# Performance work log

Measured on AMD Instinct MI355X. Metric: run time of the kernel, lower is better.

Reference implementation:

```python
import jax, jax.numpy as jnp
import numpy as np

# MLA dims (DeepSeek-V3-lite style)
B, S, DIM = 1, 2048, 2048
H, NOPE, ROPE, VD, LORA = 16, 128, 64, 128, 512
QK_HEAD = NOPE + ROPE  # 192
SCALE = QK_HEAD ** -0.5
EPS = 1e-6


def _rmsnorm(x, w):
    return x * jax.lax.rsqrt(jnp.mean(x * x, axis=-1, keepdims=True) + EPS) * w


def _apply_rope(x, cos, sin):
    # x: [b, s, h, d] with interleaved (real, imag) pairs; cos/sin: [s, d//2]
    x0, x1 = x[..., 0::2], x[..., 1::2]
    c = cos[None, :, None, :]
    s = sin[None, :, None, :]
    y0 = x0 * c - x1 * s
    y1 = x0 * s + x1 * c
    return jnp.stack([y0, y1], axis=-1).reshape(x.shape)


def setup_inputs() -> dict:
    key = jax.random.key(0)
    ks = jax.random.split(key, 6)
    x = jax.random.normal(ks[0], (B, S, DIM), jnp.float32) * 0.02
    wq = jax.random.normal(ks[1], (H * QK_HEAD, DIM), jnp.float32) * 0.02
    wkv_a = jax.random.normal(ks[2], (LORA + ROPE, DIM), jnp.float32) * 0.02
    kv_norm_w = jnp.ones((LORA,), jnp.float32)
    wkv_b = jax.random.normal(ks[3], (H * (NOPE + VD), LORA), jnp.float32) * 0.02
    wo = jax.random.normal(ks[4], (DIM, H * VD), jnp.float32) * 0.02
    # rotary freqs_cis (cos/sin) for qk_rope_head_dim
    inv_freq = 1.0 / (10000.0 ** (np.arange(0, ROPE, 2, dtype=np.float32) / ROPE))
    t = np.arange(S, dtype=np.float32)
    ang = np.outer(t, inv_freq)  # [S, ROPE//2]
    cos = jnp.asarray(np.cos(ang), jnp.float32)
    sin = jnp.asarray(np.sin(ang), jnp.float32)
    return {"x": x, "cos": cos, "sin": sin, "wq": wq, "wkv_a": wkv_a,
            "kv_norm_w": kv_norm_w, "wkv_b": wkv_b, "wo": wo}


def reference(x, cos, sin, wq, wkv_a, kv_norm_w, wkv_b, wo):
    b, s, _ = x.shape
    # queries
    q = (x @ wq.T).reshape(b, s, H, QK_HEAD)
    q_nope, q_pe = q[..., :NOPE], q[..., NOPE:]
    q_pe = _apply_rope(q_pe, cos, sin)  # [b,s,h,rope]
    # latent kv
    kv = x @ wkv_a.T  # [b,s,lora+rope]
    kv_c, k_pe = kv[..., :LORA], kv[..., LORA:]
    k_pe = _apply_rope(k_pe[:, :, None, :], cos, sin)[:, :, 0, :]  # [b,s,rope]
    kv_c = _rmsnorm(kv_c, kv_norm_w)  # latent kv cache [b,s,lora]
    # absorbed weights: wkv_b viewed as [h, nope+vd, lora]
    wkv_b_r = wkv_b.reshape(H, NOPE + VD, LORA)
    w_uk = wkv_b_r[:, :NOPE]   # [h, nope, lora]
    w_uv = wkv_b_r[:, NOPE:]   # [h, vd, lora]
    # absorb: project q_nope into latent space
    q_c = jnp.einsum('bshd,hdc->bshc', q_nope, w_uk)  # [b,s,h,lora]
    scores = (jnp.einsum('bshc,btc->bsht', q_c, kv_c)
              + jnp.einsum('bshr,btr->bsht', q_pe, k_pe)) * SCALE
    # causal mask over [s, t]
    mask = jnp.where(jnp.arange(s)[:, None] >= jnp.arange(s)[None, :], 0.0, -1e30)
    scores = scores + mask[None, :, None, :].astype(scores.dtype)
    attn = jax.nn.softmax(scores, axis=-1)
    o = jnp.einsum('bsht,btc->bshc', attn, kv_c)       # [b,s,h,lora]
    o = jnp.einsum('bshc,hdc->bshd', o, w_uv)           # [b,s,h,vd]
    out = o.reshape(b, s, H * VD) @ wo.T                # [b,s,dim]
    return out
```

## Files before the change

### kernel.cpp

```cpp
#include <hip/hip_runtime.h>
#include <hip/hip_bf16.h>
#include <math.h>

#define S_LEN 2048
#define DIM   2048
#define H_N   16
#define NOPE  128
#define ROPE  64
#define VD    128
#define LORA  512
#define D_QK  576
#define SCALE_F 0.07216878364870323f
#define EPS_F 1e-6f
#define KVF 640
#define KVS 1280

typedef short short8 __attribute__((ext_vector_type(8)));
typedef short short4v __attribute__((ext_vector_type(4)));
typedef float floatx4 __attribute__((ext_vector_type(4)));

static __device__ inline unsigned short f2bf_bits(float f) {
  union { __hip_bfloat16 h; unsigned short u; } cv;
  cv.h = __float2bfloat16(f);
  return cv.u;
}

static __device__ inline float bf2f(unsigned short b) {
  union { unsigned u; float f; } cv;
  cv.u = (unsigned)b << 16;
  return cv.f;
}

static __device__ inline void gload_lds16(const short* gptr, short* lds_base_uniform) {
  __builtin_amdgcn_global_load_lds(
      (const __attribute__((address_space(1))) void*)gptr,
      (__attribute__((address_space(3))) void*)lds_base_uniform, 16, 0, 0);
}

__global__ __launch_bounds__(256) void cast_f32_bf16(
    const float* __restrict__ src, short* __restrict__ dst, int n8) {
  int i = blockIdx.x * 256 + threadIdx.x;
  if (i < n8) {
    float4 a = ((const float4*)src)[2 * i];
    float4 b = ((const float4*)src)[2 * i + 1];
    uint4 o;
    o.x = (unsigned)f2bf_bits(a.x) | ((unsigned)f2bf_bits(a.y) << 16);
    o.y = (unsigned)f2bf_bits(a.z) | ((unsigned)f2bf_bits(a.w) << 16);
    o.z = (unsigned)f2bf_bits(b.x) | ((unsigned)f2bf_bits(b.y) << 16);
    o.w = (unsigned)f2bf_bits(b.z) | ((unsigned)f2bf_bits(b.w) << 16);
    ((uint4*)dst)[i] = o;
  }
}

__global__ __launch_bounds__(256) void zero_short8(short* __restrict__ dst, int n8) {
  int i = blockIdx.x * 256 + threadIdx.x;
  if (i < n8) ((uint4*)dst)[i] = (uint4){0u, 0u, 0u, 0u};
}

__global__ __launch_bounds__(256) void transpose_wuk(
    const float* __restrict__ wkvb, short* __restrict__ wukT) {
  __shared__ float tile[32][33];
  const int h = blockIdx.z, c0 = blockIdx.y * 32, d0 = blockIdx.x * 32;
  const int t = threadIdx.x;
  const int r = t >> 3, c4 = (t & 7) * 4;
  float4 v = *(const float4*)(wkvb + ((long)h * 256 + d0 + r) * 512 + c0 + c4);
  tile[r][c4 + 0] = v.x; tile[r][c4 + 1] = v.y;
  tile[r][c4 + 2] = v.z; tile[r][c4 + 3] = v.w;
  __syncthreads();
  uint2 o;
  o.x = (unsigned)f2bf_bits(tile[c4 + 0][r]) | ((unsigned)f2bf_bits(tile[c4 + 1][r]) << 16);
  o.y = (unsigned)f2bf_bits(tile[c4 + 2][r]) | ((unsigned)f2bf_bits(tile[c4 + 3][r]) << 16);
  *(uint2*)(wukT + ((long)h * 512 + c0 + r) * 128 + d0 + c4) = o;
}

__global__ __launch_bounds__(256) void gemm_bf16_nt(
    const short* __restrict__ A, const short* __restrict__ B, void* __restrict__ Cv,
    int K, int lda, int ldb, int ldc, long aB, long bB, long cB, int bf16out) {
  A += (long)blockIdx.z * aB;
  B += (long)blockIdx.z * bB;
  const int m0 = blockIdx.y * 128, n0 = blockIdx.x * 128;
  __shared__ short As[2][128 * 32];
  __shared__ short Bs[2][128 * 32];
  const int tid = threadIdx.x, w = tid >> 6, lane = tid & 63;
  const int ln = lane & 15, g = lane >> 4;
  const int mw = (w & 1) * 64, nw = (w >> 1) * 64;
  floatx4 acc[4][4];
#pragma unroll
  for (int i = 0; i < 4; ++i)
#pragma unroll
    for (int j = 0; j < 4; ++j) acc[i][j] = (floatx4){0.f, 0.f, 0.f, 0.f};

#define GEMM_STAGE(k0_, b_)                                                    \
  {                                                                            \
    _Pragma("unroll")                                                          \
    for (int i = 0; i < 2; ++i) {                                              \
      const int bc = (i * 4 + w) * 64;                                         \
      const int c = bc + lane;                                                 \
      const int row = c >> 2, quar = c & 3;                                    \
      gload_lds16(A + (long)(m0 + row) * lda + (k0_) + quar * 8, As[b_] + bc * 8); \
      gload_lds16(B + (long)(n0 + row) * ldb + (k0_) + quar * 8, Bs[b_] + bc * 8); \
    }                                                                          \
  }

  GEMM_STAGE(0, 0);
  __syncthreads();
  const int nk = K >> 5;
  for (int kt = 0; kt < nk; ++kt) {
    const int cb = kt & 1;
    if (kt + 1 < nk) GEMM_STAGE((kt + 1) << 5, cb ^ 1);
    short8 af[4], bf_[4];
#pragma unroll
    for (int mi = 0; mi < 4; ++mi)
      af[mi] = *(const short8*)(As[cb] + (mw + mi * 16 + ln) * 32 + g * 8);
#pragma unroll
    for (int ni = 0; ni < 4; ++ni)
      bf_[ni] = *(const short8*)(Bs[cb] + (nw + ni * 16 + ln) * 32 + g * 8);
#pragma unroll
    for (int mi = 0; mi < 4; ++mi)
#pragma unroll
      for (int ni = 0; ni < 4; ++ni)
        acc[mi][ni] = __builtin_amdgcn_mfma_f32_16x16x32_bf16(af[mi], bf_[ni], acc[mi][ni], 0, 0, 0);
    __syncthreads();
  }
#undef GEMM_STAGE
  if (bf16out) {
    short* Cs = (short*)Cv + (long)blockIdx.z * cB;
#pragma unroll
    for (int mi = 0; mi < 4; ++mi)
#pragma unroll
      for (int ni = 0; ni < 4; ++ni)
#pragma unroll
        for (int r = 0; r < 4; ++r)
          Cs[(long)(m0 + mw + mi * 16 + g * 4 + r) * ldc + n0 + nw + ni * 16 + ln] =
              (short)f2bf_bits(acc[mi][ni][r]);
  } else {
    float* C = (float*)Cv + (long)blockIdx.z * cB;
#pragma unroll
    for (int mi = 0; mi < 4; ++mi)
#pragma unroll
      for (int ni = 0; ni < 4; ++ni)
#pragma unroll
        for (int r = 0; r < 4; ++r)
          C[(long)(m0 + mw + mi * 16 + g * 4 + r) * ldc + n0 + nw + ni * 16 + ln] = acc[mi][ni][r];
  }
}

__global__ __launch_bounds__(256) void gemm_bf16_nt_m64(
    const short* __restrict__ A, const short* __restrict__ B, void* __restrict__ Cv,
    int K, int lda, int ldb, int ldc, long aB, long bB, long cB, int bf16out) {
  A += (long)blockIdx.z * aB;
  B += (long)blockIdx.z * bB;
  const int m0 = blockIdx.y * 64, n0 = blockIdx.x * 128;
  __shared__ short As[2][64 * 32];
  __shared__ short Bs[2][128 * 32];
  const int tid = threadIdx.x, w = tid >> 6, lane = tid & 63;
  const int ln = lane & 15, g = lane >> 4;
  const int mw = (w & 1) * 32, nw = (w >> 1) * 64;
  floatx4 acc[2][4];
#pragma unroll
  for (int i = 0; i < 2; ++i)
#pragma unroll
    for (int j = 0; j < 4; ++j) acc[i][j] = (floatx4){0.f, 0.f, 0.f, 0.f};

#define GEMM_STAGE64(k0_, b_)                                                  \
  {                                                                            \
    {                                                                          \
      const int bc = w * 64;                                                   \
      const int c = bc + lane;                                                 \
      const int row = c >> 2, quar = c & 3;                                    \
      gload_lds16(A + (long)(m0 + row) * lda + (k0_) + quar * 8, As[b_] + bc * 8); \
    }                                                                          \
    _Pragma("unroll")                                                          \
    for (int i = 0; i < 2; ++i) {                                              \
      const int bc = (i * 4 + w) * 64;                                         \
      const int c = bc + lane;                                                 \
      const int row = c >> 2, quar = c & 3;                                    \
      gload_lds16(B + (long)(n0 + row) * ldb + (k0_) + quar * 8, Bs[b_] + bc * 8); \
    }                                                                          \
  }

  GEMM_STAGE64(0, 0);
  __syncthreads();
  const int nk = K >> 5;
  for (int kt = 0; kt < nk; ++kt) {
    const int cb = kt & 1;
    if (kt + 1 < nk) GEMM_STAGE64((kt + 1) << 5, cb ^ 1);
    short8 af[2], bf_[4];
#pragma unroll
    for (int mi = 0; mi < 2; ++mi)
      af[mi] = *(const short8*)(As[cb] + (mw + mi * 16 + ln) * 32 + g * 8);
#pragma unroll
    for (int ni = 0; ni < 4; ++ni)
      bf_[ni] = *(const short8*)(Bs[cb] + (nw + ni * 16 + ln) * 32 + g * 8);
#pragma unroll
    for (int mi = 0; mi < 2; ++mi)
#pragma unroll
      for (int ni = 0; ni < 4; ++ni)
        acc[mi][ni] = __builtin_amdgcn_mfma_f32_16x16x32_bf16(af[mi], bf_[ni], acc[mi][ni], 0, 0, 0);
    __syncthreads();
  }
#undef GEMM_STAGE64
  if (bf16out) {
    short* Cs = (short*)Cv + (long)blockIdx.z * cB;
#pragma unroll
    for (int mi = 0; mi < 2; ++mi)
#pragma unroll
      for (int ni = 0; ni < 4; ++ni)
#pragma unroll
        for (int r = 0; r < 4; ++r)
          Cs[(long)(m0 + mw + mi * 16 + g * 4 + r) * ldc + n0 + nw + ni * 16 + ln] =
              (short)f2bf_bits(acc[mi][ni][r]);
  } else {
    float* C = (float*)Cv + (long)blockIdx.z * cB;
#pragma unroll
    for (int mi = 0; mi < 2; ++mi)
#pragma unroll
      for (int ni = 0; ni < 4; ++ni)
#pragma unroll
        for (int r = 0; r < 4; ++r)
          C[(long)(m0 + mw + mi * 16 + g * 4 + r) * ldc + n0 + nw + ni * 16 + ln] = acc[mi][ni][r];
  }
}

__global__ __launch_bounds__(64) void prep_kernel(
    float* kv, const short* __restrict__ qbufb, short* __restrict__ qhatb,
    const float* __restrict__ cosp, const float* __restrict__ sinp,
    const float* __restrict__ normw) {
  const int s = blockIdx.x;
  const int l = threadIdx.x;
  float* row = kv + (long)s * KVF;
  short* krow = (short*)kv + (long)s * KVS;

  float4 v0 = *(const float4*)(row + l * 8);
  float4 v1 = *(const float4*)(row + l * 8 + 4);
  float rx0 = 0.f, rx1 = 0.f, rc = 0.f, rs = 0.f;
  if (l < 32) {
    rc = cosp[s * 32 + l];
    rs = sinp[s * 32 + l];
    rx0 = row[512 + 2 * l];
    rx1 = row[512 + 2 * l + 1];
  }
  float4 w0 = *(const float4*)(normw + l * 8);
  float4 w1 = *(const float4*)(normw + l * 8 + 4);

  float ss = v0.x * v0.x + v0.y * v0.y + v0.z * v0.z + v0.w * v0.w +
             v1.x * v1.x + v1.y * v1.y + v1.z * v1.z + v1.w * v1.w;
#pragma unroll
  for (int off = 32; off; off >>= 1) ss += __shfl_xor(ss, off, 64);
  const float scale = rsqrtf(ss * (1.0f / (float)LORA) + EPS_F);
  v0.x *= scale * w0.x; v0.y *= scale * w0.y; v0.z *= scale * w0.z; v0.w *= scale * w0.w;
  v1.x *= scale * w1.x; v1.y *= scale * w1.y; v1.z *= scale * w1.z; v1.w *= scale * w1.w;

  uint4 pk;
  pk.x = (unsigned)f2bf_bits(v0.x) | ((unsigned)f2bf_bits(v0.y) << 16);
  pk.y = (unsigned)f2bf_bits(v0.z) | ((unsigned)f2bf_bits(v0.w) << 16);
  pk.z = (unsigned)f2bf_bits(v1.x) | ((unsigned)f2bf_bits(v1.y) << 16);
  pk.w = (unsigned)f2bf_bits(v1.z) | ((unsigned)f2bf_bits(v1.w) << 16);
  *(uint4*)(krow + l * 8) = pk;

  if (l < 32) {
    const float y0 = rx0 * rc - rx1 * rs;
    const float y1 = rx0 * rs + rx1 * rc;
    unsigned pr = (unsigned)f2bf_bits(y0) | ((unsigned)f2bf_bits(y1) << 16);
    *(unsigned*)(krow + 512 + 2 * l) = pr;
  }

#pragma unroll
  for (int it = 0; it < 8; ++it) {
    const int p = it * 64 + l;
    const int h = p >> 5;
    const int i = p & 31;
    const float c = cosp[s * 32 + i];
    const float sn = sinp[s * 32 + i];
    const short* qp = qbufb + (long)s * 3072 + h * 192 + NOPE;
    const unsigned uq = *(const unsigned*)(qp + 2 * i);
    const float x0 = bf2f((unsigned short)uq);
    const float x1 = bf2f((unsigned short)(uq >> 16));
    const float y0 = x0 * c - x1 * sn;
    const float y1 = x0 * sn + x1 * c;
    short* dst = qhatb + ((long)h * S_LEN + s) * D_QK + 512;
    *(unsigned*)(dst + 2 * i) = (unsigned)f2bf_bits(y0) | ((unsigned)f2bf_bits(y1) << 16);
  }
}

__global__ __launch_bounds__(256) void transpose_v(
    const short* __restrict__ kbf, short* __restrict__ kvt) {
  __shared__ short tile[32][36];
  const int d0 = blockIdx.x * 32;
  const int s0 = blockIdx.y * 32;
  const int t = threadIdx.x;
  const int r = t >> 3;
  const int c4 = (t & 7) * 4;
  uint2 v = *(const uint2*)(kbf + (long)(s0 + r) * KVS + d0 + c4);
  *(uint2*)(&tile[r][c4]) = v;
  __syncthreads();
  uint2 o;
  o.x = (unsigned)(unsigned short)tile[c4 + 0][r] | ((unsigned)(unsigned short)tile[c4 + 1][r] << 16);
  o.y = (unsigned)(unsigned short)tile[c4 + 2][r] | ((unsigned)(unsigned short)tile[c4 + 3][r] << 16);
  *(uint2*)(kvt + (long)(d0 + r) * S_LEN + s0 + c4) = o;
}

__global__ __launch_bounds__(256) void build_ktt(
    const short* __restrict__ kbf, short* __restrict__ ktt) {
  const int kt = blockIdx.x;
  for (int idx = threadIdx.x; idx < 18 * 64; idx += 256) {
    const int c = idx >> 6, l = idx & 63;
    const int ln = l & 15, g = l >> 4;
    uint4 v = *(const uint4*)(kbf + (long)(kt * 16 + ln) * KVS + c * 32 + g * 8);
    *(uint4*)(ktt + ((long)(kt * 18 + c) * 64 + l) * 8) = v;
  }
}

__global__ __launch_bounds__(256) void build_vtt(
    const short* __restrict__ kvt, short* __restrict__ vtt) {
  const int kt = blockIdx.x;
  for (int idx = threadIdx.x; idx < 32 * 64; idx += 256) {
    const int nt = idx >> 6, l = idx & 63;
    const int ln = l & 15, g = l >> 4;
    uint4 v = *(const uint4*)(kvt + (long)(nt * 16 + ln) * S_LEN + kt * 32 + g * 8);
    *(uint4*)(vtt + ((long)(kt * 32 + nt) * 64 + l) * 8) = v;
  }
}

__global__ __launch_bounds__(512, 2) void flash_reg(
    const short* __restrict__ qhat,
    const short* __restrict__ ktt,
    const short* __restrict__ vtt,
    short* __restrict__ obuf) {
  const int bid = blockIdx.x;
  const int hp = bid & 7;
  const int v = bid >> 3;
  const int vi = v & 31, vj = v >> 5;
  const int qt2 = (vj == 0) ? 63 - vi : vi;
  const int q0 = qt2 * 32;
  const int tid = threadIdx.x;
  const int w = tid >> 6;
  const int lane = tid & 63;
  const int ln = lane & 15, g = lane >> 4;
  const int hh = w & 1;
  const int dh = (w >> 1) & 1;
  const int qt = w >> 2;
  const int h = hp * 2 + hh;
  const int qrow = q0 + qt * 16 + ln;
  const int qlim = qrow;

  __shared__ short Kt[2][36 * 512];
  __shared__ short Vt[2][32 * 512];
  __shared__ __align__(16) short Pl[2][2][2][16][40];
  __shared__ float Ls[8][16];

  short8 qfr[18];
  {
    const short* qr = qhat + ((long)h * S_LEN + qrow) * D_QK;
#pragma unroll
    for (int c = 0; c < 18; ++c)
      qfr[c] = *(const short8*)(qr + c * 32 + g * 8);
  }

  floatx4 oacc[16];
#pragma unroll
  for (int nt = 0; nt < 16; ++nt) oacc[nt] = (floatx4){0.f, 0.f, 0.f, 0.f};
  float lsum = 0.f;

  const int npairs = qt2 + 1;

#define FL_STAGEK(pair_, b_)                                                   \
  {                                                                            \
    const short* ks_ = ktt + (long)(pair_) * (36 * 512);                       \
    _Pragma("unroll")                                                          \
    for (int i = 0; i < 5; ++i) {                                              \
      const int grp = i * 8 + w;                                               \
      if (grp < 36)                                                            \
        gload_lds16(ks_ + (long)(grp * 64 + lane) * 8, Kt[b_] + grp * 512);    \
    }                                                                          \
  }

#define FL_STAGEV(pair_, b_)                                                   \
  {                                                                            \
    const short* vs_ = vtt + (long)(pair_) * (32 * 512);                       \
    _Pragma("unroll")                                                          \
    for (int i = 0; i < 4; ++i) {                                              \
      const int grp = i * 8 + w;                                               \
      gload_lds16(vs_ + (long)(grp * 64 + lane) * 8, Vt[b_] + grp * 512);      \
    }                                                                          \
  }

#define FL_PV(par_)                                                            \
  {                                                                            \
    const short8 pb8 = *(const short8*)(&Pl[par_][hh][qt][ln][g * 8]);         \
    const short* vb_ = Vt[par_] + dh * (16 * 512);                             \
    _Pragma("unroll")                                                          \
    for (int half = 0; half < 2; ++half) {                                     \
      short8 va[8];                                                            \
      _Pragma("unroll")                                                        \
      for (int j = 0; j < 8; ++j)                                              \
        va[j] = *(const short8*)(vb_ + (half * 8 + j) * 512 + lane * 8);       \
      __builtin_amdgcn_s_setprio(1);                                           \
      _Pragma("unroll")                                                        \
      for (int j = 0; j < 8; ++j)                                              \
        oacc[half * 8 + j] = __builtin_amdgcn_mfma_f32_16x16x32_bf16(          \
            va[j], pb8, oacc[half * 8 + j], 0, 0, 0);                          \
      __builtin_amdgcn_s_setprio(0);                                           \
    }                                                                          \
  }

  FL_STAGEK(0, 0);
  __syncthreads();

  for (int p = 0; p < npairs; ++p) {
    const int cb = p & 1;
    if (p + 1 < npairs) FL_STAGEK(p + 1, cb ^ 1);
    FL_STAGEV(p, cb);
    const short* kb = Kt[cb] + dh * (18 * 512);
    floatx4 s0 = (floatx4){0.f, 0.f, 0.f, 0.f};
    floatx4 s1 = (floatx4){0.f, 0.f, 0.f, 0.f};
    __builtin_amdgcn_s_setprio(1);
#pragma unroll
    for (int c = 0; c < 18; c += 2) {
      short8 k0 = *(const short8*)(kb + (c * 64 + lane) * 8);
      short8 k1 = *(const short8*)(kb + ((c + 1) * 64 + lane) * 8);
      s0 = __builtin_amdgcn_mfma_f32_16x16x32_bf16(k0, qfr[c], s0, 0, 0, 0);
      s1 = __builtin_amdgcn_mfma_f32_16x16x32_bf16(k1, qfr[c + 1], s1, 0, 0, 0);
    }
    __builtin_amdgcn_s_setprio(0);
    short4v p4;
    float psum = 0.f;
#pragma unroll
    for (int r = 0; r < 4; ++r) {
      const int ki = p * 32 + dh * 16 + g * 4 + r;
      float sc = fminf(fmaxf((s0[r] + s1[r]) * SCALE_F, -30.f), 30.f);
      float pv_ = (ki <= qlim) ? __expf(sc) : 0.f;
      psum += pv_;
      p4[r] = (short)f2bf_bits(pv_);
    }
    lsum += psum;
    union { short4v s; unsigned long long u; } upk;
    upk.s = p4;
    *(unsigned long long*)(&Pl[cb][hh][qt][ln][dh * 16 + g * 4]) = upk.u;
    if (p > 0) FL_PV(cb ^ 1);
    __syncthreads();
  }
  FL_PV((npairs - 1) & 1);
#undef FL_PV
#undef FL_STAGEV
#undef FL_STAGEK

  lsum += __shfl_xor(lsum, 16, 64);
  lsum += __shfl_xor(lsum, 32, 64);
  if (g == 0) Ls[w][ln] = lsum;
  __syncthreads();
  lsum += Ls[w ^ 2][ln];
  const float inv = 1.0f / fmaxf(lsum, 1e-30f);

  short* orow = obuf + ((long)h * S_LEN + qrow) * 512 + dh * 256 + g * 4;
#pragma unroll
  for (int nt = 0; nt < 16; ++nt) {
    unsigned lo = (unsigned)f2bf_bits(oacc[nt][0] * inv) | ((unsigned)f2bf_bits(oacc[nt][1] * inv) << 16);
    unsigned hi = (unsigned)f2bf_bits(oacc[nt][2] * inv) | ((unsigned)f2bf_bits(oacc[nt][3] * inv) << 16);
    unsigned long long st = (unsigned long long)lo | ((unsigned long long)hi << 32);
    *(unsigned long long*)(orow + nt * 16) = st;
  }
}

extern "C" void kernel_launch(void* const* d_in, const int* in_sizes, int n_in,
                              void* d_out, int out_size, void* d_ws, size_t ws_size,
                              hipStream_t stream) {
  (void)in_sizes; (void)n_in; (void)out_size; (void)ws_size;
  const float* x      = (const float*)d_in[0];
  const float* cosp   = (const float*)d_in[1];
  const float* sinp   = (const float*)d_in[2];
  const float* wq     = (const float*)d_in[3];
  const float* wkv_a  = (const float*)d_in[4];
  const float* normw  = (const float*)d_in[5];
  const float* wkv_b  = (const float*)d_in[6];
  const float* wo     = (const float*)d_in[7];
  float* out = (float*)d_out;

  float* ws = (float*)d_ws;
  float* qbufR  = ws;
  float* kvold  = qbufR + (long)S_LEN * 3072;
  float* qhatR  = kvold + (long)S_LEN * D_QK;
  float* obufR  = qhatR + (long)H_N * S_LEN * D_QK;
  float* oprojR = obufR + (long)H_N * S_LEN * LORA;

  float* kvpad = oprojR;
  short* kbf = (short*)kvpad;
  short* wkvap = (short*)kvold;

  short* qbufb = (short*)qbufR;
  short* kvt = qbufb + (long)S_LEN * 3072;
  short* ktt = kvt + (long)512 * S_LEN;
  short* vtt = ktt + (long)128 * 18 * 64 * 8;

  short* qhatb  = (short*)qhatR;
  short* wkvbb  = qhatb + (long)H_N * S_LEN * D_QK;
  short* oprojb = wkvbb + (long)4096 * 512;
  short* wob    = oprojb + (long)2048 * 2048;

  short* xb   = (short*)obufR;
  short* wqb  = xb  + (long)2048 * 2048;
  short* wukT = wqb + (long)3072 * 2048;
  short* obufb = (short*)obufR;

  cast_f32_bf16<<<dim3(2048), 256, 0, stream>>>(x, xb, 2048 * 2048 / 8);
  cast_f32_bf16<<<dim3(3072), 256, 0, stream>>>(wq, wqb, 3072 * 2048 / 8);
  cast_f32_bf16<<<dim3(576), 256, 0, stream>>>(wkv_a, wkvap, 576 * 2048 / 8);
  zero_short8<<<dim3(64), 256, 0, stream>>>(wkvap + 576L * 2048, 64 * 2048 / 8);

  gemm_bf16_nt<<<dim3(3072 / 128, 2048 / 128, 1), 256, 0, stream>>>(
      xb, wqb, qbufb, 2048, 2048, 2048, 3072, 0, 0, 0, 1);

  gemm_bf16_nt<<<dim3(KVF / 128, 2048 / 128, 1), 256, 0, stream>>>(
      xb, wkvap, kvpad, 2048, 2048, 2048, KVF, 0, 0, 0, 0);

  prep_kernel<<<dim3(S_LEN), 64, 0, stream>>>(kvpad, qbufb, qhatb, cosp, sinp, normw);

  transpose_wuk<<<dim3(4, 16, 16), 256, 0, stream>>>(wkv_b, wukT);

  gemm_bf16_nt<<<dim3(512 / 128, 2048 / 128, 16), 256, 0, stream>>>(
      qbufb, wukT, qhatb, 128, 3072, 128, 576,
      192L, 512L * 128, (long)S_LEN * D_QK, 1);

  transpose_v<<<dim3(16, 64), 256, 0, stream>>>(kbf, kvt);
  build_ktt<<<dim3(128), 256, 0, stream>>>(kbf, ktt);
  build_vtt<<<dim3(64), 256, 0, stream>>>(kvt, vtt);

  flash_reg<<<dim3(512), 512, 0, stream>>>(qhatb, ktt, vtt, obufb);

  cast_f32_bf16<<<dim3(1024), 256, 0, stream>>>(wkv_b, wkvbb, 4096 * 512 / 8);

  gemm_bf16_nt_m64<<<dim3(1, 2048 / 64, 16), 256, 0, stream>>>(
      obufb, wkvbb + 128L * 512, oprojb, 512, 512, 512, 2048,
      (long)S_LEN * 512, 256L * 512, 128L, 1);

  cast_f32_bf16<<<dim3(2048), 256, 0, stream>>>(wo, wob, 2048 * 2048 / 8);
  gemm_bf16_nt_m64<<<dim3(2048 / 128, 2048 / 64, 1), 256, 0, stream>>>(
      oprojb, wob, out, 2048, 2048, 2048, 2048, 0, 0, 0, 0);
}
```

Baseline: 445.5 us.

## Fuse all fp32-to-bf16 casts into one kernel and merge Q/KV projection GEMMs

All weight and input casts, plus the zero padding, now run in a single segmented kernel at the start instead of five separate launches spread through the pipeline. The Q and latent-KV projections share the same input, so they are computed by one GEMM over a concatenated weight buffer with 64x128 tiles. Tiles whose columns fall in the KV range are written as fp32 to the KV buffer, the rest as bf16 to the Q buffer. The absorb GEMM also switches to the 64-row tile variant to launch more blocks. This cuts launch overhead and improves wave fill, but it relies on the bf16 weight buffers now written early not being overwritten by intermediate kernels.

```diff
diff --git a/kernel.cpp b/kernel.cpp
--- a/kernel.cpp
+++ b/kernel.cpp
@@ -37,24 +37,44 @@
       (__attribute__((address_space(3))) void*)lds_base_uniform, 16, 0, 0);
 }
 
-__global__ __launch_bounds__(256) void cast_f32_bf16(
-    const float* __restrict__ src, short* __restrict__ dst, int n8) {
+static __device__ inline void cast8(const float* __restrict__ src,
+                                    short* __restrict__ dst, int i) {
+  float4 a = ((const float4*)src)[2 * i];
+  float4 b = ((const float4*)src)[2 * i + 1];
+  uint4 o;
+  o.x = (unsigned)f2bf_bits(a.x) | ((unsigned)f2bf_bits(a.y) << 16);
+  o.y = (unsigned)f2bf_bits(a.z) | ((unsigned)f2bf_bits(a.w) << 16);
+  o.z = (unsigned)f2bf_bits(b.x) | ((unsigned)f2bf_bits(b.y) << 16);
+  o.w = (unsigned)f2bf_bits(b.z) | ((unsigned)f2bf_bits(b.w) << 16);
+  ((uint4*)dst)[i] = o;
+}
+
+#define CSEG0 524288
+#define CSEG1 (CSEG0 + 786432)
+#define CSEG2 (CSEG1 + 147456)
+#define CSEG3 (CSEG2 + 16384)
+#define CSEG4 (CSEG3 + 262144)
+#define CSEG5 (CSEG4 + 524288)
+__global__ __launch_bounds__(256) void cast_all(
+    const float* __restrict__ x, const float* __restrict__ wq,
+    const float* __restrict__ wkv_a, const float* __restrict__ wkv_b,
+    const float* __restrict__ wo, short* __restrict__ xb,
+    short* __restrict__ wcat, short* __restrict__ wkvbb,
+    short* __restrict__ wob) {
   int i = blockIdx.x * 256 + threadIdx.x;
-  if (i < n8) {
-    float4 a = ((const float4*)src)[2 * i];
-    float4 b = ((const float4*)src)[2 * i + 1];
-    uint4 o;
-    o.x = (unsigned)f2bf_bits(a.x) | ((unsigned)f2bf_bits(a.y) << 16);
-    o.y = (unsigned)f2bf_bits(a.z) | ((unsigned)f2bf_bits(a.w) << 16);
-    o.z = (unsigned)f2bf_bits(b.x) | ((unsigned)f2bf_bits(b.y) << 16);
-    o.w = (unsigned)f2bf_bits(b.z) | ((unsigned)f2bf_bits(b.w) << 16);
-    ((uint4*)dst)[i] = o;
-  }
-}
-
-__global__ __launch_bounds__(256) void zero_short8(short* __restrict__ dst, int n8) {
-  int i = blockIdx.x * 256 + threadIdx.x;
-  if (i < n8) ((uint4*)dst)[i] = (uint4){0u, 0u, 0u, 0u};
+  if (i < CSEG0) {
+    cast8(x, xb, i);
+  } else if (i < CSEG1) {
+    cast8(wq, wcat, i - CSEG0);
+  } else if (i < CSEG2) {
+    cast8(wkv_a, wcat + 3072 * 2048, i - CSEG1);
+  } else if (i < CSEG3) {
+    ((uint4*)(wcat + 3072 * 2048 + 576 * 2048))[i - CSEG2] = (uint4){0u, 0u, 0u, 0u};
+  } else if (i < CSEG4) {
+    cast8(wkv_b, wkvbb, i - CSEG3);
+  } else if (i < CSEG5) {
+    cast8(wo, wob, i - CSEG4);
+  }
 }
 
 __global__ __launch_bounds__(256) void transpose_wuk(
@@ -73,78 +93,6 @@
   *(uint2*)(wukT + ((long)h * 512 + c0 + r) * 128 + d0 + c4) = o;
 }
 
-__global__ __launch_bounds__(256) void gemm_bf16_nt(
-    const short* __restrict__ A, const short* __restrict__ B, void* __restrict__ Cv,
-    int K, int lda, int ldb, int ldc, long aB, long bB, long cB, int bf16out) {
-  A += (long)blockIdx.z * aB;
-  B += (long)blockIdx.z * bB;
-  const int m0 = blockIdx.y * 128, n0 = blockIdx.x * 128;
-  __shared__ short As[2][128 * 32];
-  __shared__ short Bs[2][128 * 32];
-  const int tid = threadIdx.x, w = tid >> 6, lane = tid & 63;
-  const int ln = lane & 15, g = lane >> 4;
-  const int mw = (w & 1) * 64, nw = (w >> 1) * 64;
-  floatx4 acc[4][4];
-#pragma unroll
-  for (int i = 0; i < 4; ++i)
-#pragma unroll
-    for (int j = 0; j < 4; ++j) acc[i][j] = (floatx4){0.f, 0.f, 0.f, 0.f};
-
-#define GEMM_STAGE(k0_, b_)                                                    \
-  {                                                                            \
-    _Pragma("unroll")                                                          \
-    for (int i = 0; i < 2; ++i) {                                              \
-      const int bc = (i * 4 + w) * 64;                                         \
-      const int c = bc + lane;                                                 \
-      const int row = c >> 2, quar = c & 3;                                    \
-      gload_lds16(A + (long)(m0 + row) * lda + (k0_) + quar * 8, As[b_] + bc * 8); \
-      gload_lds16(B + (long)(n0 + row) * ldb + (k0_) + quar * 8, Bs[b_] + bc * 8); \
-    }                                                                          \
-  }
-
-  GEMM_STAGE(0, 0);
-  __syncthreads();
-  const int nk = K >> 5;
-  for (int kt = 0; kt < nk; ++kt) {
-    const int cb = kt & 1;
-    if (kt + 1 < nk) GEMM_STAGE((kt + 1) << 5, cb ^ 1);
-    short8 af[4], bf_[4];
-#pragma unroll
-    for (int mi = 0; mi < 4; ++mi)
-      af[mi] = *(const short8*)(As[cb] + (mw + mi * 16 + ln) * 32 + g * 8);
-#pragma unroll
-    for (int ni = 0; ni < 4; ++ni)
-      bf_[ni] = *(const short8*)(Bs[cb] + (nw + ni * 16 + ln) * 32 + g * 8);
-#pragma unroll
-    for (int mi = 0; mi < 4; ++mi)
-#pragma unroll
-      for (int ni = 0; ni < 4; ++ni)
-        acc[mi][ni] = __builtin_amdgcn_mfma_f32_16x16x32_bf16(af[mi], bf_[ni], acc[mi][ni], 0, 0, 0);
-    __syncthreads();
-  }
-#undef GEMM_STAGE
-  if (bf16out) {
-    short* Cs = (short*)Cv + (long)blockIdx.z * cB;
-#pragma unroll
-    for (int mi = 0; mi < 4; ++mi)
-#pragma unroll
-      for (int ni = 0; ni < 4; ++ni)
-#pragma unroll
-        for (int r = 0; r < 4; ++r)
-          Cs[(long)(m0 + mw + mi * 16 + g * 4 + r) * ldc + n0 + nw + ni * 16 + ln] =
-              (short)f2bf_bits(acc[mi][ni][r]);
-  } else {
-    float* C = (float*)Cv + (long)blockIdx.z * cB;
-#pragma unroll
-    for (int mi = 0; mi < 4; ++mi)
-#pragma unroll
-      for (int ni = 0; ni < 4; ++ni)
-#pragma unroll
-        for (int r = 0; r < 4; ++r)
-          C[(long)(m0 + mw + mi * 16 + g * 4 + r) * ldc + n0 + nw + ni * 16 + ln] = acc[mi][ni][r];
-  }
-}
-
 __global__ __launch_bounds__(256) void gemm_bf16_nt_m64(
     const short* __restrict__ A, const short* __restrict__ B, void* __restrict__ Cv,
     int K, int lda, int ldb, int ldc, long aB, long bB, long cB, int bf16out) {
@@ -219,6 +167,79 @@
 #pragma unroll
         for (int r = 0; r < 4; ++r)
           C[(long)(m0 + mw + mi * 16 + g * 4 + r) * ldc + n0 + nw + ni * 16 + ln] = acc[mi][ni][r];
+  }
+}
+
+__global__ __launch_bounds__(256) void gemm_qkv_m64(
+    const short* __restrict__ A, const short* __restrict__ B,
+    short* __restrict__ Cq, float* __restrict__ Ckv) {
+  const int m0 = blockIdx.y * 64, n0 = blockIdx.x * 128;
+  __shared__ short As[2][64 * 32];
+  __shared__ short Bs[2][128 * 32];
+  const int tid = threadIdx.x, w = tid >> 6, lane = tid & 63;
+  const int ln = lane & 15, g = lane >> 4;
+  const int mw = (w & 1) * 32, nw = (w >> 1) * 64;
+  floatx4 acc[2][4];
+#pragma unroll
+  for (int i = 0; i < 2; ++i)
+#pragma unroll
+    for (int j = 0; j < 4; ++j) acc[i][j] = (floatx4){0.f, 0.f, 0.f, 0.f};
+
+#define QKV_STAGE(k0_, b_)                                                     \
+  {                                                                            \
+    {                                                                          \
+      const int bc = w * 64;                                                   \
+      const int c = bc + lane;                                                 \
+      const int row = c >> 2, quar = c & 3;                                    \
+      gload_lds16(A + (long)(m0 + row) * 2048 + (k0_) + quar * 8, As[b_] + bc * 8); \
+    }                                                                          \
+    _Pragma("unroll")                                                          \
+    for (int i = 0; i < 2; ++i) {                                              \
+      const int bc = (i * 4 + w) * 64;                                         \
+      const int c = bc + lane;                                                 \
+      const int row = c >> 2, quar = c & 3;                                    \
+      gload_lds16(B + (long)(n0 + row) * 2048 + (k0_) + quar * 8, Bs[b_] + bc * 8); \
+    }                                                                          \
+  }
+
+  QKV_STAGE(0, 0);
+  __syncthreads();
+  for (int kt = 0; kt < 64; ++kt) {
+    const int cb = kt & 1;
+    if (kt + 1 < 64) QKV_STAGE((kt + 1) << 5, cb ^ 1);
+    short8 af[2], bf_[4];
+#pragma unroll
+    for (int mi = 0; mi < 2; ++mi)
+      af[mi] = *(const short8*)(As[cb] + (mw + mi * 16 + ln) * 32 + g * 8);
+#pragma unroll
+    for (int ni = 0; ni < 4; ++ni)
+      bf_[ni] = *(const short8*)(Bs[cb] + (nw + ni * 16 + ln) * 32 + g * 8);
+#pragma unroll
+    for (int mi = 0; mi < 2; ++mi)
+#pragma unroll
+      for (int ni = 0; ni < 4; ++ni)
+        acc[mi][ni] = __builtin_amdgcn_mfma_f32_16x16x32_bf16(af[mi], bf_[ni], acc[mi][ni], 0, 0, 0);
+    __syncthreads();
+  }
+#undef QKV_STAGE
+  if (n0 < 3072) {
+#pragma unroll
+    for (int mi = 0; mi < 2; ++mi)
+#pragma unroll
+      for (int ni = 0; ni < 4; ++ni)
+#pragma unroll
+        for (int r = 0; r < 4; ++r)
+          Cq[(long)(m0 + mw + mi * 16 + g * 4 + r) * 3072 + n0 + nw + ni * 16 + ln] =
+              (short)f2bf_bits(acc[mi][ni][r]);
+  } else {
+#pragma unroll
+    for (int mi = 0; mi < 2; ++mi)
+#pragma unroll
+      for (int ni = 0; ni < 4; ++ni)
+#pragma unroll
+        for (int r = 0; r < 4; ++r)
+          Ckv[(long)(m0 + mw + mi * 16 + g * 4 + r) * KVF + (n0 - 3072) + nw + ni * 16 + ln] =
+              acc[mi][ni][r];
   }
 }
 
@@ -485,7 +506,6 @@
 
   float* kvpad = oprojR;
   short* kbf = (short*)kvpad;
-  short* wkvap = (short*)kvold;
 
   short* qbufb = (short*)qbufR;
   short* kvt = qbufb + (long)S_LEN * 3072;
@@ -498,26 +518,21 @@
   short* wob    = oprojb + (long)2048 * 2048;
 
   short* xb   = (short*)obufR;
-  short* wqb  = xb  + (long)2048 * 2048;
-  short* wukT = wqb + (long)3072 * 2048;
+  short* wcat = xb + (long)2048 * 2048;
+  short* wukT = wcat + (long)3712 * 2048;
   short* obufb = (short*)obufR;
 
-  cast_f32_bf16<<<dim3(2048), 256, 0, stream>>>(x, xb, 2048 * 2048 / 8);
-  cast_f32_bf16<<<dim3(3072), 256, 0, stream>>>(wq, wqb, 3072 * 2048 / 8);
-  cast_f32_bf16<<<dim3(576), 256, 0, stream>>>(wkv_a, wkvap, 576 * 2048 / 8);
-  zero_short8<<<dim3(64), 256, 0, stream>>>(wkvap + 576L * 2048, 64 * 2048 / 8);
-
-  gemm_bf16_nt<<<dim3(3072 / 128, 2048 / 128, 1), 256, 0, stream>>>(
-      xb, wqb, qbufb, 2048, 2048, 2048, 3072, 0, 0, 0, 1);
-
-  gemm_bf16_nt<<<dim3(KVF / 128, 2048 / 128, 1), 256, 0, stream>>>(
-      xb, wkvap, kvpad, 2048, 2048, 2048, KVF, 0, 0, 0, 0);
+  cast_all<<<dim3(CSEG5 / 256), 256, 0, stream>>>(
+      x, wq, wkv_a, wkv_b, wo, xb, wcat, wkvbb, wob);
+
+  gemm_qkv_m64<<<dim3(3712 / 128, 2048 / 64, 1), 256, 0, stream>>>(
+      xb, wcat, qbufb, kvpad);
 
   prep_kernel<<<dim3(S_LEN), 64, 0, stream>>>(kvpad, qbufb, qhatb, cosp, sinp, normw);
 
   transpose_wuk<<<dim3(4, 16, 16), 256, 0, stream>>>(wkv_b, wukT);
 
-  gemm_bf16_nt<<<dim3(512 / 128, 2048 / 128, 16), 256, 0, stream>>>(
+  gemm_bf16_nt_m64<<<dim3(512 / 128, 2048 / 64, 16), 256, 0, stream>>>(
       qbufb, wukT, qhatb, 128, 3072, 128, 576,
       192L, 512L * 128, (long)S_LEN * D_QK, 1);
 
@@ -527,13 +542,10 @@
 
   flash_reg<<<dim3(512), 512, 0, stream>>>(qhatb, ktt, vtt, obufb);
 
-  cast_f32_bf16<<<dim3(1024), 256, 0, stream>>>(wkv_b, wkvbb, 4096 * 512 / 8);
-
   gemm_bf16_nt_m64<<<dim3(1, 2048 / 64, 16), 256, 0, stream>>>(
       obufb, wkvbb + 128L * 512, oprojb, 512, 512, 512, 2048,
       (long)S_LEN * 512, 256L * 512, 128L, 1);
 
-  cast_f32_bf16<<<dim3(2048), 256, 0, stream>>>(wo, wob, 2048 * 2048 / 8);
   gemm_bf16_nt_m64<<<dim3(2048 / 128, 2048 / 64, 1), 256, 0, stream>>>(
       oprojb, wob, out, 2048, 2048, 2048, 2048, 0, 0, 0, 0);
 }
```

Result: faster. 404.4 us (-9.2%).
